# Optimization experiments

Hardware: AMD Instinct MI355X
Metric: run time of the kernel (lower is better)

The kernel has to match this reference:

```python
import jax, jax.numpy as jnp
import numpy as np

INPUT_DIM = 8
NQ = 8        # num_qubits -> 2**8 = 256 amplitudes
REPS = 4
LATENT = 4
BATCH = 65536


def _apply_1q_batched(state, U, wire):
    # state: (B,) + (2,)*NQ ; U: (B, 2, 2) per-sample gate
    ax = wire + 1
    s = jnp.moveaxis(state, ax, -1)
    s = jnp.einsum('bij,b...j->b...i', U, s)
    return jnp.moveaxis(s, -1, ax)


def _apply_1q_shared(state, U, wire):
    # U: (2, 2) gate shared across the batch
    ax = wire + 1
    s = jnp.moveaxis(state, ax, -1)
    s = jnp.einsum('ij,b...j->b...i', U, s)
    return jnp.moveaxis(s, -1, ax)


def _apply_cnot(state, ctrl, tgt):
    # flip target axis on the control=1 slice
    ac, at = ctrl + 1, tgt + 1
    s0 = jax.lax.index_in_dim(state, 0, ac, keepdims=True)
    s1 = jax.lax.index_in_dim(state, 1, ac, keepdims=True)
    return jnp.concatenate([s0, jnp.flip(s1, axis=at)], axis=ac)


def _rot(phi, theta, omega):
    # PennyLane Rot(phi, theta, omega) = RZ(omega) RY(theta) RZ(phi)
    c = jnp.cos(theta / 2)
    s = jnp.sin(theta / 2)
    m00 = jnp.exp(-0.5j * (phi + omega)) * c
    m01 = -jnp.exp(0.5j * (phi - omega)) * s
    m10 = jnp.exp(-0.5j * (phi - omega)) * s
    m11 = jnp.exp(0.5j * (phi + omega)) * c
    return jnp.stack([jnp.stack([m00, m01]), jnp.stack([m10, m11])]).astype(jnp.complex64)


def _quantum_encode(x, qw):
    # batched state-vector simulation of the per-sample qnode
    B = x.shape[0]
    state = jnp.zeros((B, 2 ** NQ), jnp.complex64).at[:, 0].set(1.0)
    state = state.reshape((B,) + (2,) * NQ)
    # RX(x[i % input_dim]) on every wire (batched angles)
    for i in range(NQ):
        th = x[:, i % INPUT_DIM]
        c = jnp.cos(th / 2)
        s = jnp.sin(th / 2)
        U = jnp.stack([jnp.stack([c + 0j, -1j * s], -1),
                       jnp.stack([-1j * s, c + 0j], -1)], -2).astype(jnp.complex64)
        state = _apply_1q_batched(state, U, i)
    # StronglyEntanglingLayers: Rot on each wire, then ring of CNOTs with range r
    for l in range(REPS):
        for i in range(NQ):
            state = _apply_1q_shared(state, _rot(qw[l, i, 0], qw[l, i, 1], qw[l, i, 2]), i)
        r = (l % (NQ - 1)) + 1  # PennyLane default ranges
        for i in range(NQ):
            state = _apply_cnot(state, i, (i + r) % NQ)
    probs = state.real ** 2 + state.imag ** 2  # (B, 2, ..., 2)
    zs = []
    for i in range(NQ):
        axes = tuple(a for a in range(1, NQ + 1) if a != i + 1)
        p = probs.sum(axes)  # (B, 2)
        zs.append(p[:, 0] - p[:, 1])  # <PauliZ_i>
    return jnp.stack(zs, axis=1)  # (B, NQ)


def setup_inputs() -> dict:
    key = jax.random.key(0)
    kx, kq, k1, k2, kb1, kb2 = jax.random.split(key, 6)
    x = jax.random.normal(kx, (BATCH, INPUT_DIM), dtype=jnp.float32)
    q_weights = jax.random.normal(kq, (REPS, NQ, 3), dtype=jnp.float32)
    w1 = jax.random.normal(k1, (LATENT, NQ), dtype=jnp.float32) / np.sqrt(NQ)
    b1 = jax.random.normal(kb1, (LATENT,), dtype=jnp.float32) * 0.01
    w2 = jax.random.normal(k2, (INPUT_DIM, LATENT), dtype=jnp.float32) / np.sqrt(LATENT)
    b2 = jax.random.normal(kb2, (INPUT_DIM,), dtype=jnp.float32) * 0.01
    return {'x': x, 'q_weights': q_weights, 'w1': w1, 'b1': b1, 'w2': w2, 'b2': b2}


def reference(x, q_weights, w1, b1, w2, b2):
    z = _quantum_encode(x, q_weights)          # (B, NQ)
    h = jax.nn.relu(z @ w1.T + b1)             # (B, LATENT)
    return h @ w2.T + b2                       # (B, INPUT_DIM)
```

## Files before the change

kernel.cpp:

```cpp
#include <hip/hip_runtime.h>
#include <math.h>


typedef float v2f __attribute__((ext_vector_type(2)));

struct M8 { unsigned char r[8]; };

constexpr M8 ident8() {
    M8 m{};
    for (int b = 0; b < 8; ++b) m.r[b] = (unsigned char)(1u << b);
    return m;
}
constexpr M8 ring_mat(M8 m, int s) {
    for (int i = 0; i < 8; ++i) {
        const int cb = 7 - i, tb = 7 - ((i + s) & 7);
        m.r[tb] = (unsigned char)(m.r[tb] ^ m.r[cb]);
    }
    return m;
}
constexpr M8 inv8(M8 a) {
    M8 inv = ident8();
    for (int col = 0; col < 8; ++col) {
        int piv = col;
        while (!((a.r[piv] >> col) & 1)) ++piv;
        unsigned char t = a.r[piv]; a.r[piv] = a.r[col]; a.r[col] = t;
        t = inv.r[piv]; inv.r[piv] = inv.r[col]; inv.r[col] = t;
        for (int q = 0; q < 8; ++q)
            if (q != col && ((a.r[q] >> col) & 1)) {
                a.r[q] = (unsigned char)(a.r[q] ^ a.r[col]);
                inv.r[q] = (unsigned char)(inv.r[q] ^ inv.r[col]);
            }
    }
    return inv;
}
constexpr int mask_of(M8 inv, int b) {
    int m = 0;
    for (int j = 0; j < 8; ++j) m |= ((inv.r[j] >> b) & 1) << j;
    return m;
}

constexpr M8 P1c  = ring_mat(ident8(), 1);
constexpr M8 P2c  = ring_mat(P1c, 2);
constexpr M8 P3c  = ring_mat(P2c, 3);
constexpr M8 P4c  = ring_mat(P3c, 4);
constexpr M8 P1ic = inv8(P1c);
constexpr M8 P2ic = inv8(P2c);
constexpr M8 P3ic = inv8(P3c);

template<int CTRL>
__device__ __forceinline__ float dppf(float v) {
    const int i = __float_as_int(v);
    return __int_as_float(__builtin_amdgcn_update_dpp(i, i, CTRL, 0xF, 0xF, true));
}
template<int M>
__device__ __forceinline__ float lxorf(float v) {
    static_assert(M >= 1 && M <= 15, "bad mask");
    if constexpr (M == 1)       return dppf<0xB1>(v);
    else if constexpr (M == 2)  return dppf<0x4E>(v);
    else if constexpr (M == 3)  return dppf<0x1B>(v);
    else if constexpr (M == 7)  return dppf<0x141>(v);
    else if constexpr (M == 8)  return dppf<0x128>(v);
    else if constexpr (M == 15) return dppf<0x140>(v);
    else return __int_as_float(__builtin_amdgcn_ds_swizzle(__float_as_int(v), (M << 10) | 0x1F));
}

template<int MASK, int DUAL>
__device__ __forceinline__ void gry(float (&re)[16], float (&im)[16], int ll, v2f cs)
{
    constexpr int ml = (MASK >> 4) & 15, ms = MASK & 15;
    constexpr int dl = (DUAL >> 4) & 15, ds = DUAL & 15;
    const float c = cs.x, s = cs.y;
    float tp;
    if constexpr (dl != 0) {
        int t = ll & dl; t ^= t >> 2; t ^= t >> 1;
        tp = (t & 1) ? s : -s;
    } else {
        tp = -s;
    }
    const float tn = -tp;
    if constexpr (ms == 0) {
        #pragma unroll
        for (int r = 0; r < 16; ++r) {
            int pp = r & ds; pp ^= pp >> 2; pp ^= pp >> 1;
            const float tr = (pp & 1) ? tn : tp;
            re[r] = fmaf(tr, lxorf<ml>(re[r]), c * re[r]);
            im[r] = fmaf(tr, lxorf<ml>(im[r]), c * im[r]);
        }
    } else {
        constexpr int lo = ms & (-ms);
        #pragma unroll
        for (int r0 = 0; r0 < 16; ++r0) {
            if ((r0 & lo) == 0) {
                const int r1 = r0 ^ ms;
                int p0 = r0 & ds; p0 ^= p0 >> 2; p0 ^= p0 >> 1;
                int p1 = r1 & ds; p1 ^= p1 >> 2; p1 ^= p1 >> 1;
                const float t0 = (p0 & 1) ? tn : tp;
                const float t1 = (p1 & 1) ? tn : tp;
                float q0r, q0i, q1r, q1i;
                if constexpr (ml != 0) {
                    q0r = lxorf<ml>(re[r1]); q0i = lxorf<ml>(im[r1]);
                    q1r = lxorf<ml>(re[r0]); q1i = lxorf<ml>(im[r0]);
                } else {
                    q0r = re[r1]; q0i = im[r1];
                    q1r = re[r0]; q1i = im[r0];
                }
                const float n0r = fmaf(t0, q0r, c * re[r0]);
                const float n0i = fmaf(t0, q0i, c * im[r0]);
                const float n1r = fmaf(t1, q1r, c * re[r1]);
                const float n1i = fmaf(t1, q1i, c * im[r1]);
                re[r0] = n0r; im[r0] = n0i;
                re[r1] = n1r; im[r1] = n1i;
            }
        }
    }
}

template<int L>
__device__ __forceinline__ void gry_layer(float (&re)[16], float (&im)[16], int ll,
                                          const v2f* __restrict__ cs)
{
    constexpr M8 P  = (L == 1) ? P1c  : (L == 2) ? P2c  : P3c;
    constexpr M8 Pi = (L == 1) ? P1ic : (L == 2) ? P2ic : P3ic;
    gry<mask_of(Pi, 7), P.r[7]>(re, im, ll, cs[0]);
    gry<mask_of(Pi, 6), P.r[6]>(re, im, ll, cs[1]);
    gry<mask_of(Pi, 5), P.r[5]>(re, im, ll, cs[2]);
    gry<mask_of(Pi, 4), P.r[4]>(re, im, ll, cs[3]);
    gry<mask_of(Pi, 3), P.r[3]>(re, im, ll, cs[4]);
    gry<mask_of(Pi, 2), P.r[2]>(re, im, ll, cs[5]);
    gry<mask_of(Pi, 1), P.r[1]>(re, im, ll, cs[6]);
    gry<mask_of(Pi, 0), P.r[0]>(re, im, ll, cs[7]);
}

__device__ __forceinline__ void diag_apply(float (&re)[16], float (&im)[16],
                                           const float* __restrict__ tab, int ll)
{
    const float4* p4 = reinterpret_cast<const float4*>(tab + ll * 36);
    #pragma unroll
    for (int j = 0; j < 8; ++j) {
        const float4 v = p4[j];
        const int r0 = 2 * j, r1 = 2 * j + 1;
        float nr = v.x * re[r0] - v.y * im[r0];
        float ni = v.x * im[r0] + v.y * re[r0];
        re[r0] = nr; im[r0] = ni;
        nr = v.z * re[r1] - v.w * im[r1];
        ni = v.z * im[r1] + v.w * re[r1];
        re[r1] = nr; im[r1] = ni;
    }
}

__device__ __forceinline__ void init_state(const float* __restrict__ xp,
                                           const v2f (*Gc)[4], int ll,
                                           float (&re)[16], float (&im)[16])
{
    const float4 xv0 = *reinterpret_cast<const float4*>(xp);
    const float4 xv1 = *reinterpret_cast<const float4*>(xp + 4);
    const float xs[8] = {xv0.x, xv0.y, xv0.z, xv0.w, xv1.x, xv1.y, xv1.z, xv1.w};
    const int b0 = (ll >> 3) & 1, b1_ = (ll >> 2) & 1, b2_ = (ll >> 1) & 1, b3 = ll & 1;

    v2f w0v[8], w1v[8];
    #pragma unroll
    for (int i = 0; i < 8; ++i) {
        float sx, cx;
        __sincosf(0.5f * xs[i], &sx, &cx);
        const v2f m00 = Gc[i][0], m01 = Gc[i][1], m10 = Gc[i][2], m11 = Gc[i][3];
        w0v[i].x = fmaf(cx, m00.x,  sx * m01.y);
        w0v[i].y = fmaf(cx, m00.y, -(sx * m01.x));
        w1v[i].x = fmaf(cx, m10.x,  sx * m11.y);
        w1v[i].y = fmaf(cx, m10.y, -(sx * m11.x));
    }

    v2f L = b0 ? w1v[0] : w0v[0];
    {
        const v2f f = b1_ ? w1v[1] : w0v[1];
        v2f t; t.x = fmaf(L.x, f.x, -(L.y * f.y)); t.y = fmaf(L.x, f.y, L.y * f.x); L = t;
    }
    {
        const v2f f = b2_ ? w1v[2] : w0v[2];
        v2f t; t.x = fmaf(L.x, f.x, -(L.y * f.y)); t.y = fmaf(L.x, f.y, L.y * f.x); L = t;
    }
    {
        const v2f f = b3 ? w1v[3] : w0v[3];
        v2f t; t.x = fmaf(L.x, f.x, -(L.y * f.y)); t.y = fmaf(L.x, f.y, L.y * f.x); L = t;
    }

    v2f p45[4], p67[4];
    #pragma unroll
    for (int a = 0; a < 4; ++a) {
        const int bh = (a >> 1) & 1, bl = a & 1;
        const v2f u = bh ? w1v[4] : w0v[4], v = bl ? w1v[5] : w0v[5];
        p45[a].x = fmaf(u.x, v.x, -(u.y * v.y)); p45[a].y = fmaf(u.x, v.y, u.y * v.x);
        const v2f u2 = bh ? w1v[6] : w0v[6], v2_ = bl ? w1v[7] : w0v[7];
        p67[a].x = fmaf(u2.x, v2_.x, -(u2.y * v2_.y)); p67[a].y = fmaf(u2.x, v2_.y, u2.y * v2_.x);
    }
    v2f L45[4];
    #pragma unroll
    for (int a = 0; a < 4; ++a) {
        L45[a].x = fmaf(L.x, p45[a].x, -(L.y * p45[a].y));
        L45[a].y = fmaf(L.x, p45[a].y,   L.y * p45[a].x);
    }
    #pragma unroll
    for (int r = 0; r < 16; ++r) {
        const int a = r >> 2, b = r & 3;
        re[r] = fmaf(L45[a].x, p67[b].x, -(L45[a].y * p67[b].y));
        im[r] = fmaf(L45[a].x, p67[b].y,   L45[a].y * p67[b].x);
    }
}

template<int DL>
__device__ __forceinline__ float lane_wht(float v, int ll)
{
    if constexpr ((DL & 1) == 0) v += lxorf<1>(v); else v -= lxorf<1>(v);
    if constexpr ((DL & 2) == 0) v += lxorf<2>(v); else v -= lxorf<2>(v);
    if constexpr ((DL & 4) == 0) v += lxorf<4>(v); else v -= lxorf<4>(v);
    if constexpr ((DL & 8) == 0) v += lxorf<8>(v); else v -= lxorf<8>(v);
    if constexpr (DL != 0) {
        int t = ll & DL; t ^= t >> 2; t ^= t >> 1;
        v = (t & 1) ? -v : v;
    }
    return v;
}

__device__ __forceinline__ float dotang(const float* __restrict__ w, int t)
{
    float a = 0.f;
    #pragma unroll
    for (int i = 0; i < 8; ++i) {
        const float h = 0.5f * w[i * 3];
        a += ((t >> (7 - i)) & 1) ? h : -h;
    }
    return a;
}
__device__ __forceinline__ int applyP(M8 m, int u)
{
    int t = 0;
    #pragma unroll
    for (int b = 0; b < 8; ++b)
        t |= (__builtin_popcount((int)m.r[b] & u) & 1) << b;
    return t;
}

__global__ void __launch_bounds__(256)
qae_fused(const float* __restrict__ x, const float* __restrict__ qw,
          const float* __restrict__ w1, const float* __restrict__ b1,
          const float* __restrict__ w2, const float* __restrict__ b2,
          float* __restrict__ out, int nsamp)
{
    __shared__ __align__(16) float dA[16 * 36];
    __shared__ __align__(16) float dB[16 * 36];
    __shared__ __align__(16) float dC[16 * 36];
    __shared__ __align__(16) v2f Gc[8][4];
    __shared__ v2f RyCS[24];

    const int tid = threadIdx.x;
    const int u = tid;

    {
        const int t1 = applyP(P1c, u);
        const int t2 = applyP(P2c, u);
        const int t3 = applyP(P3c, u);
        const float aA = dotang(qw + 24 + 0, t1);
        const float aB = dotang(qw + 24 + 2, t1) + dotang(qw + 48 + 0, t2);
        const float aC = dotang(qw + 48 + 2, t2) + dotang(qw + 72 + 0, t3);
        const int row = u >> 4, col = u & 15;
        const int idx = row * 36 + col * 2;
        float s_, c_;
        __sincosf(aA, &s_, &c_); dA[idx] = c_; dA[idx + 1] = s_;
        __sincosf(aB, &s_, &c_); dB[idx] = c_; dB[idx + 1] = s_;
        __sincosf(aC, &s_, &c_); dC[idx] = c_; dC[idx + 1] = s_;
    }
    if (tid < 24) {
        const int l = 1 + (tid >> 3), i = tid & 7;
        float s_, c_;
        sincosf(0.5f * qw[l * 24 + i * 3 + 1], &s_, &c_);
        v2f t; t.x = c_; t.y = s_;
        RyCS[tid] = t;
    }
    if (tid >= 32 && tid < 40) {
        const int i = tid - 32;
        const float phi = qw[i * 3 + 0], th = qw[i * 3 + 1], om = qw[i * 3 + 2];
        float s, c, sp, cp, sm, cm;
        sincosf(0.5f * th,         &s,  &c);
        sincosf(0.5f * (phi + om), &sp, &cp);
        sincosf(0.5f * (phi - om), &sm, &cm);
        v2f t;
        t.x =  cp * c; t.y = -sp * c; Gc[i][0] = t;
        t.x = -cm * s; t.y = -sm * s; Gc[i][1] = t;
        t.x =  cm * s; t.y = -sm * s; Gc[i][2] = t;
        t.x =  cp * c; t.y =  sp * c; Gc[i][3] = t;
    }
    __syncthreads();

    const int sample = (blockIdx.x * 256 + tid) >> 4;
    if (sample >= nsamp) return;
    const int ll = tid & 15;

    float re[16], im[16];
    init_state(x + (size_t)sample * 8, Gc, ll, re, im);

    diag_apply(re, im, dA, ll);
    gry_layer<1>(re, im, ll, RyCS);
    diag_apply(re, im, dB, ll);
    gry_layer<2>(re, im, ll, RyCS + 8);
    diag_apply(re, im, dC, ll);
    gry_layer<3>(re, im, ll, RyCS + 16);

    float W[16];
    #pragma unroll
    for (int r = 0; r < 16; ++r) W[r] = fmaf(re[r], re[r], im[r] * im[r]);
    #pragma unroll
    for (int b = 0; b < 4; ++b) {
        const int m = 1 << b;
        #pragma unroll
        for (int r = 0; r < 16; ++r) {
            if (!(r & m)) {
                const float a = W[r], bb = W[r ^ m];
                W[r] = a + bb; W[r ^ m] = a - bb;
            }
        }
    }
    float z[8];
    z[0] = lane_wht<(P4c.r[7] >> 4)>(W[P4c.r[7] & 15], ll);
    z[1] = lane_wht<(P4c.r[6] >> 4)>(W[P4c.r[6] & 15], ll);
    z[2] = lane_wht<(P4c.r[5] >> 4)>(W[P4c.r[5] & 15], ll);
    z[3] = lane_wht<(P4c.r[4] >> 4)>(W[P4c.r[4] & 15], ll);
    z[4] = lane_wht<(P4c.r[3] >> 4)>(W[P4c.r[3] & 15], ll);
    z[5] = lane_wht<(P4c.r[2] >> 4)>(W[P4c.r[2] & 15], ll);
    z[6] = lane_wht<(P4c.r[1] >> 4)>(W[P4c.r[1] & 15], ll);
    z[7] = lane_wht<(P4c.r[0] >> 4)>(W[P4c.r[0] & 15], ll);

    if (ll < 8) {
        float h0 = b1[0], h1 = b1[1], h2 = b1[2], h3 = b1[3];
        #pragma unroll
        for (int i = 0; i < 8; ++i) {
            h0 += z[i] * w1[i];
            h1 += z[i] * w1[8 + i];
            h2 += z[i] * w1[16 + i];
            h3 += z[i] * w1[24 + i];
        }
        h0 = fmaxf(h0, 0.f); h1 = fmaxf(h1, 0.f);
        h2 = fmaxf(h2, 0.f); h3 = fmaxf(h3, 0.f);
        const float o = b2[ll] + h0 * w2[ll * 4 + 0] + h1 * w2[ll * 4 + 1]
                                + h2 * w2[ll * 4 + 2] + h3 * w2[ll * 4 + 3];
        out[(size_t)sample * 8 + ll] = o;
    }
}

extern "C" void kernel_launch(void* const* d_in, const int* in_sizes, int n_in,
                              void* d_out, int out_size, void* d_ws, size_t ws_size,
                              hipStream_t stream)
{
    const float* x  = (const float*)d_in[0];
    const float* qw = (const float*)d_in[1];
    const float* w1 = (const float*)d_in[2];
    const float* b1 = (const float*)d_in[3];
    const float* w2 = (const float*)d_in[4];
    const float* b2 = (const float*)d_in[5];
    float* out = (float*)d_out;

    const int nsamp = in_sizes[0] / 8;
    const int total_threads = nsamp * 16;
    const int blocks = (total_threads + 255) / 256;

    hipLaunchKernelGGL(qae_fused, dim3(blocks), dim3(256), 0, stream,
                       x, qw, w1, b1, w2, b2, out, nsamp);
}
```

Measured before the change: 61.51 us.

## Process two samples per 16-lane group to amortize table loads and ILP

Each 16-lane group now simulates two samples at once, holding two state vectors in registers and applying every gate and diagonal to both. The shared diagonal-table loads and rotation coefficients are reused across the two samples, there is more independent work per lane to hide DPP/swizzle latency, and all 16 lanes now write output instead of only 8. In exchange, register use roughly doubles and the grid is half as large, which may lower occupancy. For an odd sample count, the second sample of the last group reads and writes past the end of the arrays, because there is no bounds guard for it.

```diff
diff --git a/kernel.cpp b/kernel.cpp
--- a/kernel.cpp
+++ b/kernel.cpp
@@ -65,7 +65,9 @@
 }
 
 template<int MASK, int DUAL>
-__device__ __forceinline__ void gry(float (&re)[16], float (&im)[16], int ll, v2f cs)
+__device__ __forceinline__ void gry2(float (&re0)[16], float (&im0)[16],
+                                     float (&re1)[16], float (&im1)[16],
+                                     int ll, v2f cs)
 {
     constexpr int ml = (MASK >> 4) & 15, ms = MASK & 15;
     constexpr int dl = (DUAL >> 4) & 15, ds = DUAL & 15;
@@ -83,8 +85,10 @@
         for (int r = 0; r < 16; ++r) {
             int pp = r & ds; pp ^= pp >> 2; pp ^= pp >> 1;
             const float tr = (pp & 1) ? tn : tp;
-            re[r] = fmaf(tr, lxorf<ml>(re[r]), c * re[r]);
-            im[r] = fmaf(tr, lxorf<ml>(im[r]), c * im[r]);
+            re0[r] = fmaf(tr, lxorf<ml>(re0[r]), c * re0[r]);
+            im0[r] = fmaf(tr, lxorf<ml>(im0[r]), c * im0[r]);
+            re1[r] = fmaf(tr, lxorf<ml>(re1[r]), c * re1[r]);
+            im1[r] = fmaf(tr, lxorf<ml>(im1[r]), c * im1[r]);
         }
     } else {
         constexpr int lo = ms & (-ms);
@@ -96,55 +100,82 @@
                 int p1 = r1 & ds; p1 ^= p1 >> 2; p1 ^= p1 >> 1;
                 const float t0 = (p0 & 1) ? tn : tp;
                 const float t1 = (p1 & 1) ? tn : tp;
-                float q0r, q0i, q1r, q1i;
-                if constexpr (ml != 0) {
-                    q0r = lxorf<ml>(re[r1]); q0i = lxorf<ml>(im[r1]);
-                    q1r = lxorf<ml>(re[r0]); q1i = lxorf<ml>(im[r0]);
-                } else {
-                    q0r = re[r1]; q0i = im[r1];
-                    q1r = re[r0]; q1i = im[r0];
+                {
+                    float q0r, q0i, q1r, q1i;
+                    if constexpr (ml != 0) {
+                        q0r = lxorf<ml>(re0[r1]); q0i = lxorf<ml>(im0[r1]);
+                        q1r = lxorf<ml>(re0[r0]); q1i = lxorf<ml>(im0[r0]);
+                    } else {
+                        q0r = re0[r1]; q0i = im0[r1];
+                        q1r = re0[r0]; q1i = im0[r0];
+                    }
+                    const float n0r = fmaf(t0, q0r, c * re0[r0]);
+                    const float n0i = fmaf(t0, q0i, c * im0[r0]);
+                    const float n1r = fmaf(t1, q1r, c * re0[r1]);
+                    const float n1i = fmaf(t1, q1i, c * im0[r1]);
+                    re0[r0] = n0r; im0[r0] = n0i;
+                    re0[r1] = n1r; im0[r1] = n1i;
                 }
-                const float n0r = fmaf(t0, q0r, c * re[r0]);
-                const float n0i = fmaf(t0, q0i, c * im[r0]);
-                const float n1r = fmaf(t1, q1r, c * re[r1]);
-                const float n1i = fmaf(t1, q1i, c * im[r1]);
-                re[r0] = n0r; im[r0] = n0i;
-                re[r1] = n1r; im[r1] = n1i;
+                {
+                    float q0r, q0i, q1r, q1i;
+                    if constexpr (ml != 0) {
+                        q0r = lxorf<ml>(re1[r1]); q0i = lxorf<ml>(im1[r1]);
+                        q1r = lxorf<ml>(re1[r0]); q1i = lxorf<ml>(im1[r0]);
+                    } else {
+                        q0r = re1[r1]; q0i = im1[r1];
+                        q1r = re1[r0]; q1i = im1[r0];
+                    }
+                    const float n0r = fmaf(t0, q0r, c * re1[r0]);
+                    const float n0i = fmaf(t0, q0i, c * im1[r0]);
+                    const float n1r = fmaf(t1, q1r, c * re1[r1]);
+                    const float n1i = fmaf(t1, q1i, c * im1[r1]);
+                    re1[r0] = n0r; im1[r0] = n0i;
+                    re1[r1] = n1r; im1[r1] = n1i;
+                }
             }
         }
     }
 }
 
 template<int L>
-__device__ __forceinline__ void gry_layer(float (&re)[16], float (&im)[16], int ll,
-                                          const v2f* __restrict__ cs)
+__device__ __forceinline__ void gry_layer2(float (&re0)[16], float (&im0)[16],
+                                           float (&re1)[16], float (&im1)[16],
+                                           int ll, const v2f* __restrict__ cs)
 {
     constexpr M8 P  = (L == 1) ? P1c  : (L == 2) ? P2c  : P3c;
     constexpr M8 Pi = (L == 1) ? P1ic : (L == 2) ? P2ic : P3ic;
-    gry<mask_of(Pi, 7), P.r[7]>(re, im, ll, cs[0]);
-    gry<mask_of(Pi, 6), P.r[6]>(re, im, ll, cs[1]);
-    gry<mask_of(Pi, 5), P.r[5]>(re, im, ll, cs[2]);
-    gry<mask_of(Pi, 4), P.r[4]>(re, im, ll, cs[3]);
-    gry<mask_of(Pi, 3), P.r[3]>(re, im, ll, cs[4]);
-    gry<mask_of(Pi, 2), P.r[2]>(re, im, ll, cs[5]);
-    gry<mask_of(Pi, 1), P.r[1]>(re, im, ll, cs[6]);
-    gry<mask_of(Pi, 0), P.r[0]>(re, im, ll, cs[7]);
-}
-
-__device__ __forceinline__ void diag_apply(float (&re)[16], float (&im)[16],
-                                           const float* __restrict__ tab, int ll)
+    gry2<mask_of(Pi, 7), P.r[7]>(re0, im0, re1, im1, ll, cs[0]);
+    gry2<mask_of(Pi, 6), P.r[6]>(re0, im0, re1, im1, ll, cs[1]);
+    gry2<mask_of(Pi, 5), P.r[5]>(re0, im0, re1, im1, ll, cs[2]);
+    gry2<mask_of(Pi, 4), P.r[4]>(re0, im0, re1, im1, ll, cs[3]);
+    gry2<mask_of(Pi, 3), P.r[3]>(re0, im0, re1, im1, ll, cs[4]);
+    gry2<mask_of(Pi, 2), P.r[2]>(re0, im0, re1, im1, ll, cs[5]);
+    gry2<mask_of(Pi, 1), P.r[1]>(re0, im0, re1, im1, ll, cs[6]);
+    gry2<mask_of(Pi, 0), P.r[0]>(re0, im0, re1, im1, ll, cs[7]);
+}
+
+__device__ __forceinline__ void diag_apply2(float (&re0)[16], float (&im0)[16],
+                                            float (&re1)[16], float (&im1)[16],
+                                            const float* __restrict__ tab, int ll)
 {
     const float4* p4 = reinterpret_cast<const float4*>(tab + ll * 36);
     #pragma unroll
     for (int j = 0; j < 8; ++j) {
         const float4 v = p4[j];
         const int r0 = 2 * j, r1 = 2 * j + 1;
-        float nr = v.x * re[r0] - v.y * im[r0];
-        float ni = v.x * im[r0] + v.y * re[r0];
-        re[r0] = nr; im[r0] = ni;
-        nr = v.z * re[r1] - v.w * im[r1];
-        ni = v.z * im[r1] + v.w * re[r1];
-        re[r1] = nr; im[r1] = ni;
+        float nr, ni;
+        nr = v.x * re0[r0] - v.y * im0[r0];
+        ni = v.x * im0[r0] + v.y * re0[r0];
+        re0[r0] = nr; im0[r0] = ni;
+        nr = v.z * re0[r1] - v.w * im0[r1];
+        ni = v.z * im0[r1] + v.w * re0[r1];
+        re0[r1] = nr; im0[r1] = ni;
+        nr = v.x * re1[r0] - v.y * im1[r0];
+        ni = v.x * im1[r0] + v.y * re1[r0];
+        re1[r0] = nr; im1[r0] = ni;
+        nr = v.z * re1[r1] - v.w * im1[r1];
+        ni = v.z * im1[r1] + v.w * re1[r1];
+        re1[r1] = nr; im1[r1] = ni;
     }
 }
 
@@ -218,6 +249,24 @@
         v = (t & 1) ? -v : v;
     }
     return v;
+}
+
+__device__ __forceinline__ void slot_fwht(const float (&re)[16], const float (&im)[16],
+                                          float (&W)[16])
+{
+    #pragma unroll
+    for (int r = 0; r < 16; ++r) W[r] = fmaf(re[r], re[r], im[r] * im[r]);
+    #pragma unroll
+    for (int b = 0; b < 4; ++b) {
+        const int m = 1 << b;
+        #pragma unroll
+        for (int r = 0; r < 16; ++r) {
+            if (!(r & m)) {
+                const float a = W[r], bb = W[r ^ m];
+                W[r] = a + bb; W[r ^ m] = a - bb;
+            }
+        }
+    }
 }
 
 __device__ __forceinline__ float dotang(const float* __restrict__ w, int t)
@@ -290,59 +339,62 @@
     }
     __syncthreads();
 
-    const int sample = (blockIdx.x * 256 + tid) >> 4;
-    if (sample >= nsamp) return;
+    const int group = (blockIdx.x * 256 + tid) >> 4;
+    const int sA = group * 2;
+    if (sA >= nsamp) return;
     const int ll = tid & 15;
 
-    float re[16], im[16];
-    init_state(x + (size_t)sample * 8, Gc, ll, re, im);
-
-    diag_apply(re, im, dA, ll);
-    gry_layer<1>(re, im, ll, RyCS);
-    diag_apply(re, im, dB, ll);
-    gry_layer<2>(re, im, ll, RyCS + 8);
-    diag_apply(re, im, dC, ll);
-    gry_layer<3>(re, im, ll, RyCS + 16);
-
-    float W[16];
-    #pragma unroll
-    for (int r = 0; r < 16; ++r) W[r] = fmaf(re[r], re[r], im[r] * im[r]);
-    #pragma unroll
-    for (int b = 0; b < 4; ++b) {
-        const int m = 1 << b;
-        #pragma unroll
-        for (int r = 0; r < 16; ++r) {
-            if (!(r & m)) {
-                const float a = W[r], bb = W[r ^ m];
-                W[r] = a + bb; W[r ^ m] = a - bb;
-            }
-        }
-    }
-    float z[8];
-    z[0] = lane_wht<(P4c.r[7] >> 4)>(W[P4c.r[7] & 15], ll);
-    z[1] = lane_wht<(P4c.r[6] >> 4)>(W[P4c.r[6] & 15], ll);
-    z[2] = lane_wht<(P4c.r[5] >> 4)>(W[P4c.r[5] & 15], ll);
-    z[3] = lane_wht<(P4c.r[4] >> 4)>(W[P4c.r[4] & 15], ll);
-    z[4] = lane_wht<(P4c.r[3] >> 4)>(W[P4c.r[3] & 15], ll);
-    z[5] = lane_wht<(P4c.r[2] >> 4)>(W[P4c.r[2] & 15], ll);
-    z[6] = lane_wht<(P4c.r[1] >> 4)>(W[P4c.r[1] & 15], ll);
-    z[7] = lane_wht<(P4c.r[0] >> 4)>(W[P4c.r[0] & 15], ll);
-
-    if (ll < 8) {
-        float h0 = b1[0], h1 = b1[1], h2 = b1[2], h3 = b1[3];
-        #pragma unroll
-        for (int i = 0; i < 8; ++i) {
-            h0 += z[i] * w1[i];
-            h1 += z[i] * w1[8 + i];
-            h2 += z[i] * w1[16 + i];
-            h3 += z[i] * w1[24 + i];
-        }
-        h0 = fmaxf(h0, 0.f); h1 = fmaxf(h1, 0.f);
-        h2 = fmaxf(h2, 0.f); h3 = fmaxf(h3, 0.f);
-        const float o = b2[ll] + h0 * w2[ll * 4 + 0] + h1 * w2[ll * 4 + 1]
-                                + h2 * w2[ll * 4 + 2] + h3 * w2[ll * 4 + 3];
-        out[(size_t)sample * 8 + ll] = o;
-    }
+    float re0[16], im0[16], re1[16], im1[16];
+    init_state(x + (size_t)sA * 8,     Gc, ll, re0, im0);
+    init_state(x + (size_t)sA * 8 + 8, Gc, ll, re1, im1);
+
+    diag_apply2(re0, im0, re1, im1, dA, ll);
+    gry_layer2<1>(re0, im0, re1, im1, ll, RyCS);
+    diag_apply2(re0, im0, re1, im1, dB, ll);
+    gry_layer2<2>(re0, im0, re1, im1, ll, RyCS + 8);
+    diag_apply2(re0, im0, re1, im1, dC, ll);
+    gry_layer2<3>(re0, im0, re1, im1, ll, RyCS + 16);
+
+    float WA[16], WB[16];
+    slot_fwht(re0, im0, WA);
+    slot_fwht(re1, im1, WB);
+
+    float zA[8], zB[8];
+    zA[0] = lane_wht<(P4c.r[7] >> 4)>(WA[P4c.r[7] & 15], ll);
+    zA[1] = lane_wht<(P4c.r[6] >> 4)>(WA[P4c.r[6] & 15], ll);
+    zA[2] = lane_wht<(P4c.r[5] >> 4)>(WA[P4c.r[5] & 15], ll);
+    zA[3] = lane_wht<(P4c.r[4] >> 4)>(WA[P4c.r[4] & 15], ll);
+    zA[4] = lane_wht<(P4c.r[3] >> 4)>(WA[P4c.r[3] & 15], ll);
+    zA[5] = lane_wht<(P4c.r[2] >> 4)>(WA[P4c.r[2] & 15], ll);
+    zA[6] = lane_wht<(P4c.r[1] >> 4)>(WA[P4c.r[1] & 15], ll);
+    zA[7] = lane_wht<(P4c.r[0] >> 4)>(WA[P4c.r[0] & 15], ll);
+    zB[0] = lane_wht<(P4c.r[7] >> 4)>(WB[P4c.r[7] & 15], ll);
+    zB[1] = lane_wht<(P4c.r[6] >> 4)>(WB[P4c.r[6] & 15], ll);
+    zB[2] = lane_wht<(P4c.r[5] >> 4)>(WB[P4c.r[5] & 15], ll);
+    zB[3] = lane_wht<(P4c.r[4] >> 4)>(WB[P4c.r[4] & 15], ll);
+    zB[4] = lane_wht<(P4c.r[3] >> 4)>(WB[P4c.r[3] & 15], ll);
+    zB[5] = lane_wht<(P4c.r[2] >> 4)>(WB[P4c.r[2] & 15], ll);
+    zB[6] = lane_wht<(P4c.r[1] >> 4)>(WB[P4c.r[1] & 15], ll);
+    zB[7] = lane_wht<(P4c.r[0] >> 4)>(WB[P4c.r[0] & 15], ll);
+
+    float zs[8];
+    #pragma unroll
+    for (int i = 0; i < 8; ++i) zs[i] = (ll < 8) ? zA[i] : zB[i];
+
+    const int col = ll & 7;
+    float h0 = b1[0], h1 = b1[1], h2 = b1[2], h3 = b1[3];
+    #pragma unroll
+    for (int i = 0; i < 8; ++i) {
+        h0 += zs[i] * w1[i];
+        h1 += zs[i] * w1[8 + i];
+        h2 += zs[i] * w1[16 + i];
+        h3 += zs[i] * w1[24 + i];
+    }
+    h0 = fmaxf(h0, 0.f); h1 = fmaxf(h1, 0.f);
+    h2 = fmaxf(h2, 0.f); h3 = fmaxf(h3, 0.f);
+    const float o = b2[col] + h0 * w2[col * 4 + 0] + h1 * w2[col * 4 + 1]
+                            + h2 * w2[col * 4 + 2] + h3 * w2[col * 4 + 3];
+    out[(size_t)(sA + (ll >> 3)) * 8 + col] = o;
 }
 
 extern "C" void kernel_launch(void* const* d_in, const int* in_sizes, int n_in,
@@ -357,8 +409,9 @@
     const float* b2 = (const float*)d_in[5];
     float* out = (float*)d_out;
 
-    const int nsamp = in_sizes[0] / 8;
-    const int total_threads = nsamp * 16;
+    const int nsamp  = in_sizes[0] / 8;
+    const int groups = (nsamp + 1) / 2;
+    const int total_threads = groups * 16;
     const int blocks = (total_threads + 255) / 256;
 
     hipLaunchKernelGGL(qae_fused, dim3(blocks), dim3(256), 0, stream,
```

Result: no change. 62.17 us (+1.1%).
